# Performance work log

Measured on AMD Instinct MI355X. Metric: run time of the kernel, lower is better.

Reference implementation:

```python
import jax, jax.numpy as jnp
import numpy as np
import math

DIM = 1024
HEADS = 16
HEAD_DIM = DIM // HEADS
B, N = 1, 4096


def setup_inputs() -> dict:
    key = jax.random.key(0)
    k1, k2, k3, k4 = jax.random.split(key, 4)
    content = jax.random.normal(k1, (B, N, DIM), dtype=jnp.float32)
    # Original initializes projections as identity; perturb slightly so the
    # projections are non-trivial while staying well-conditioned.
    Wq = jnp.eye(DIM, dtype=jnp.float32) + 0.02 * jax.random.normal(k2, (DIM, DIM), dtype=jnp.float32)
    Wk = jnp.eye(DIM, dtype=jnp.float32) + 0.02 * jax.random.normal(k3, (DIM, DIM), dtype=jnp.float32)
    Wv = jnp.eye(DIM, dtype=jnp.float32) + 0.02 * jax.random.normal(k4, (DIM, DIM), dtype=jnp.float32)
    return {"content": content, "Wq": Wq, "Wk": Wk, "Wv": Wv}


def reference(content, Wq, Wk, Wv):
    b, n, d = content.shape
    # QKV projections: [B,N,D] @ [D,D]
    Q = (content @ Wq).reshape(b, n, HEADS, HEAD_DIM)
    K = (content @ Wk).reshape(b, n, HEADS, HEAD_DIM)
    V = (content @ Wv).reshape(b, n, HEADS, HEAD_DIM)
    # torch.split along the last dim == reshape into [.., HEADS, HEAD_DIM]
    scores = jnp.einsum('bqhd,bkhd->bhqk', Q, K) / math.sqrt(HEAD_DIM)
    alpha = jax.nn.softmax(scores, axis=-1)
    # Faithful to the original: masking zeroes the upper triangle AFTER the
    # softmax (no renormalization). With B=1 this applies to the whole batch,
    # exactly as the original loop (which only touches batch index 0).
    causal = jnp.tril(jnp.ones((n, n), dtype=bool))
    alpha = jnp.where(causal, alpha, jnp.zeros((), dtype=alpha.dtype))
    Y = jnp.einsum('bhqk,bkhd->bqhd', alpha, V).reshape(b, n, d)
    return Y
```

## Files before the change

### kernel.cpp

```cpp
#include <hip/hip_runtime.h>
#include <stdint.h>

#define DIMC 1024
#define NSEQ 4096
#define NH 16
#define QSCALE 0.18033688011112042f

typedef __attribute__((ext_vector_type(8))) short bf16x8;
typedef __attribute__((ext_vector_type(4))) float f32x4;

__device__ __forceinline__ unsigned short f2bf(float x) {
    union { float f; unsigned int u; } v; v.f = x;
    unsigned int u = v.u;
    return (unsigned short)((u + 0x7fffu + ((u >> 16) & 1u)) >> 16);
}

__device__ __forceinline__ unsigned cvt_pk_bf16(float lo, float hi) {
    unsigned r;
    asm("v_cvt_pk_bf16_f32 %0, %1, %2" : "=v"(r) : "v"(lo), "v"(hi));
    return r;
}

__device__ __forceinline__ void gload16(const unsigned short* g, unsigned short* l) {
    __builtin_amdgcn_global_load_lds(
        (const __attribute__((address_space(1))) void*)g,
        (__attribute__((address_space(3))) void*)l, 16, 0, 0);
}

__global__ __launch_bounds__(256) void k_conv(const float* __restrict__ in,
                                              unsigned short* __restrict__ out) {
    int i = (blockIdx.x * 256 + threadIdx.x) * 8;
    float4 a = *reinterpret_cast<const float4*>(in + i);
    float4 b = *reinterpret_cast<const float4*>(in + i + 4);
    union { unsigned short us[8]; uint4 v; } r;
    r.us[0] = f2bf(a.x); r.us[1] = f2bf(a.y); r.us[2] = f2bf(a.z); r.us[3] = f2bf(a.w);
    r.us[4] = f2bf(b.x); r.us[5] = f2bf(b.y); r.us[6] = f2bf(b.z); r.us[7] = f2bf(b.w);
    *reinterpret_cast<uint4*>(out + i) = r.v;
}

__global__ __launch_bounds__(1024) void k_wt(const float* __restrict__ Wq,
                                             const float* __restrict__ Wk,
                                             const float* __restrict__ Wv,
                                             unsigned short* __restrict__ wt) {
    __shared__ float tile[32][33];
    int z = blockIdx.z;
    const float* W = (z == 0) ? Wq : ((z == 1) ? Wk : Wv);
    int n0 = blockIdx.x * 32, k0 = blockIdx.y * 32;
    tile[threadIdx.y][threadIdx.x] = W[(k0 + threadIdx.y) * DIMC + n0 + threadIdx.x];
    __syncthreads();
    wt[(size_t)z * DIMC * DIMC + (n0 + threadIdx.y) * DIMC + k0 + threadIdx.x] =
        f2bf(tile[threadIdx.x][threadIdx.y]);
}

__global__ __launch_bounds__(256) void k_gemm(const unsigned short* __restrict__ A,
                                              const unsigned short* __restrict__ Wt,
                                              unsigned short* __restrict__ Qb,
                                              unsigned short* __restrict__ Kb,
                                              unsigned short* __restrict__ Vt) {
    __shared__ unsigned short As[128 * 32];
    __shared__ unsigned short Bs[128 * 32];
    const int z = blockIdx.z;
    const unsigned short* Wz = Wt + (size_t)z * DIMC * DIMC;
    const int n0 = blockIdx.x * 128, m0 = blockIdx.y * 128;
    const int t = threadIdx.x;
    const int w = t >> 6, l = t & 63;
    const int wr = w >> 1, wc = w & 1;
    const int lq = l & 15, lg = l >> 4;
    const int srow = l >> 2, scol = (l & 3) * 8;
    const unsigned short* gA = A  + (size_t)(m0 + w * 32 + srow) * DIMC + scol;
    const unsigned short* gB = Wz + (size_t)(n0 + w * 32 + srow) * DIMC + scol;
    unsigned short* lA = &As[(2 * w) * 512];
    unsigned short* lB = &Bs[(2 * w) * 512];

    f32x4 acc[4][4];
    #pragma unroll
    for (int i = 0; i < 4; ++i)
        #pragma unroll
        for (int j = 0; j < 4; ++j)
            acc[i][j] = f32x4{0.f, 0.f, 0.f, 0.f};

    for (int k0 = 0; k0 < DIMC; k0 += 32) {
        __syncthreads();
        gload16(gA + k0, lA);
        gload16(gA + k0 + 16 * DIMC, lA + 512);
        gload16(gB + k0, lB);
        gload16(gB + k0 + 16 * DIMC, lB + 512);
        __syncthreads();
        bf16x8 af[4], bfr[4];
        #pragma unroll
        for (int mf = 0; mf < 4; ++mf)
            af[mf] = *reinterpret_cast<const bf16x8*>(&As[(wr * 64 + mf * 16 + lq) * 32 + lg * 8]);
        #pragma unroll
        for (int nf = 0; nf < 4; ++nf)
            bfr[nf] = *reinterpret_cast<const bf16x8*>(&Bs[(wc * 64 + nf * 16 + lq) * 32 + lg * 8]);
        __builtin_amdgcn_s_setprio(1);
        #pragma unroll
        for (int mf = 0; mf < 4; ++mf)
            #pragma unroll
            for (int nf = 0; nf < 4; ++nf)
                acc[mf][nf] = __builtin_amdgcn_mfma_f32_16x16x32_bf16(af[mf], bfr[nf], acc[mf][nf], 0, 0, 0);
        __builtin_amdgcn_s_setprio(0);
    }

    if (z < 2) {
        unsigned short* out = (z == 0) ? Qb : Kb;
        const float osc = (z == 0) ? QSCALE : 1.0f;
        #pragma unroll
        for (int mf = 0; mf < 4; ++mf)
            #pragma unroll
            for (int nf = 0; nf < 4; ++nf)
                #pragma unroll
                for (int j = 0; j < 4; ++j) {
                    int row = m0 + wr * 64 + mf * 16 + lg * 4 + j;
                    int col = n0 + wc * 64 + nf * 16 + lq;
                    out[row * DIMC + col] = f2bf(acc[mf][nf][j] * osc);
                }
    } else {
        #pragma unroll
        for (int mf = 0; mf < 4; ++mf)
            #pragma unroll
            for (int nf = 0; nf < 4; ++nf) {
                int row  = n0 + wc * 64 + nf * 16 + lq;
                int colb = m0 + wr * 64 + mf * 16 + lg * 4;
                uint2 pk;
                pk.x = cvt_pk_bf16(acc[mf][nf][0], acc[mf][nf][1]);
                pk.y = cvt_pk_bf16(acc[mf][nf][2], acc[mf][nf][3]);
                *reinterpret_cast<uint2*>(Vt + (size_t)row * NSEQ + colb) = pk;
            }
    }
}

__global__ __launch_bounds__(512, 4) void k_attn(const unsigned short* __restrict__ Qb,
                                                 const unsigned short* __restrict__ Kb,
                                                 const unsigned short* __restrict__ Vt,
                                                 float* __restrict__ Y) {
    __shared__ unsigned short Ks[64][72];
    __shared__ unsigned short Vs[64][72];
    __shared__ unsigned short Ps[8][16][88];
    const int bx = blockIdx.x, h = blockIdx.y;
    const int t = threadIdx.x;
    const int w = t >> 6, l = t & 63;
    const int wq = w & 3, tile = w >> 2;
    const int lq = l & 15, lg = l >> 4;
    const int qbA = bx, qbB = 63 - bx;
    const int qb_my = tile ? qbB : qbA;

    bf16x8 qf0, qf1;
    {
        const unsigned short* qp = Qb + (size_t)(qb_my * 64 + wq * 16 + lq) * DIMC + h * 64 + lg * 8;
        qf0 = *reinterpret_cast<const bf16x8*>(qp);
        qf1 = *reinterpret_cast<const bf16x8*>(qp + 32);
    }
    float m_fr = -__builtin_inff(), l_st = 0.f;
    f32x4 O[4];
    #pragma unroll
    for (int df = 0; df < 4; ++df) O[df] = f32x4{0.f, 0.f, 0.f, 0.f};

    const int r0 = t >> 3, c0 = (t & 7) * 8;
    const unsigned short* gK = Kb + (size_t)r0 * DIMC + h * 64 + c0;
    const unsigned short* gV = Vt + (size_t)(h * 64 + r0) * NSEQ + c0;

    uint4 kv = *reinterpret_cast<const uint4*>(gK);
    uint4 vv = *reinterpret_cast<const uint4*>(gV);

    for (int kt = 0; kt < 64; ++kt) {
        __syncthreads();
        *reinterpret_cast<uint4*>(&Ks[r0][c0]) = kv;
        if (kt <= qbB) *reinterpret_cast<uint4*>(&Vs[r0][c0]) = vv;
        __syncthreads();
        if (kt < 63) {
            kv = *reinterpret_cast<const uint4*>(gK + (size_t)(kt + 1) * 64 * DIMC);
            if (kt + 1 <= qbB) vv = *reinterpret_cast<const uint4*>(gV + (kt + 1) * 64);
        }

        f32x4 s[4];
        __builtin_amdgcn_s_setprio(1);
        #pragma unroll
        for (int f = 0; f < 4; ++f) {
            s[f] = f32x4{0.f, 0.f, 0.f, 0.f};
            bf16x8 ka0 = *reinterpret_cast<const bf16x8*>(&Ks[f * 16 + lq][lg * 8]);
            bf16x8 ka1 = *reinterpret_cast<const bf16x8*>(&Ks[f * 16 + lq][32 + lg * 8]);
            s[f] = __builtin_amdgcn_mfma_f32_16x16x32_bf16(ka0, qf0, s[f], 0, 0, 0);
            s[f] = __builtin_amdgcn_mfma_f32_16x16x32_bf16(ka1, qf1, s[f], 0, 0, 0);
        }
        __builtin_amdgcn_s_setprio(0);

        float tmax = s[0][0];
        #pragma unroll
        for (int f = 0; f < 4; ++f)
            #pragma unroll
            for (int j = 0; j < 4; ++j) tmax = fmaxf(tmax, s[f][j]);
        tmax = fmaxf(tmax, __shfl_xor(tmax, 16));
        tmax = fmaxf(tmax, __shfl_xor(tmax, 32));

        if (!__all(tmax <= m_fr + 8.f)) {
            const float mnew = fmaxf(m_fr, tmax);
            const float sc = exp2f(m_fr - mnew);
            l_st *= sc;
            #pragma unroll
            for (int j = 0; j < 4; ++j) {
                const float scj = __shfl(sc, lg * 4 + j);
                #pragma unroll
                for (int df = 0; df < 4; ++df) O[df][j] *= scj;
            }
            m_fr = mnew;
        }
        float psum = 0.f;
        #pragma unroll
        for (int f = 0; f < 4; ++f)
            #pragma unroll
            for (int j = 0; j < 4; ++j) {
                const float p = exp2f(s[f][j] - m_fr);
                s[f][j] = p;
                psum += p;
            }
        psum += __shfl_xor(psum, 16);
        psum += __shfl_xor(psum, 32);
        l_st += psum;

        if (kt <= qb_my) {
            if (kt == qb_my) {
                const int qrel = wq * 16 + lq;
                #pragma unroll
                for (int f = 0; f < 4; ++f) {
                    const int kbase = f * 16 + lg * 4;
                    #pragma unroll
                    for (int j = 0; j < 4; ++j)
                        if (kbase + j > qrel) s[f][j] = 0.f;
                }
            }
            #pragma unroll
            for (int f = 0; f < 4; ++f) {
                uint2 pk;
                pk.x = cvt_pk_bf16(s[f][0], s[f][1]);
                pk.y = cvt_pk_bf16(s[f][2], s[f][3]);
                *reinterpret_cast<uint2*>(&Ps[w][lq][f * 16 + lg * 4]) = pk;
            }
            __builtin_amdgcn_s_setprio(1);
            #pragma unroll
            for (int kk = 0; kk < 2; ++kk) {
                bf16x8 pa = *reinterpret_cast<const bf16x8*>(&Ps[w][lq][kk * 32 + lg * 8]);
                #pragma unroll
                for (int df = 0; df < 4; ++df) {
                    bf16x8 vb = *reinterpret_cast<const bf16x8*>(&Vs[df * 16 + lq][kk * 32 + lg * 8]);
                    O[df] = __builtin_amdgcn_mfma_f32_16x16x32_bf16(pa, vb, O[df], 0, 0, 0);
                }
            }
            __builtin_amdgcn_s_setprio(0);
        }
    }

    const float rl = 1.0f / l_st;
    #pragma unroll
    for (int j = 0; j < 4; ++j) {
        const float li = __shfl(rl, lg * 4 + j);
        #pragma unroll
        for (int df = 0; df < 4; ++df)
            Y[(qb_my * 64 + wq * 16 + lg * 4 + j) * DIMC + h * 64 + df * 16 + lq] = O[df][j] * li;
    }
}

extern "C" void kernel_launch(void* const* d_in, const int* in_sizes, int n_in,
                              void* d_out, int out_size, void* d_ws, size_t ws_size,
                              hipStream_t stream) {
    const float* content = (const float*)d_in[0];
    const float* Wq = (const float*)d_in[1];
    const float* Wk = (const float*)d_in[2];
    const float* Wv = (const float*)d_in[3];
    float* Y = (float*)d_out;
    unsigned short* ws  = (unsigned short*)d_ws;
    unsigned short* cbf = ws;
    unsigned short* wt  = cbf + (size_t)NSEQ * DIMC;
    unsigned short* qb  = wt  + (size_t)3 * DIMC * DIMC;
    unsigned short* kb  = qb  + (size_t)NSEQ * DIMC;
    unsigned short* vt  = kb  + (size_t)NSEQ * DIMC;

    hipLaunchKernelGGL(k_conv, dim3(NSEQ * DIMC / (256 * 8)), dim3(256), 0, stream, content, cbf);
    hipLaunchKernelGGL(k_wt,   dim3(32, 32, 3), dim3(32, 32), 0, stream, Wq, Wk, Wv, wt);
    hipLaunchKernelGGL(k_gemm, dim3(DIMC / 128, NSEQ / 128, 3), dim3(256), 0, stream, cbf, wt, qb, kb, vt);
    hipLaunchKernelGGL(k_attn, dim3(NSEQ / 128, NH), dim3(512), 0, stream, qb, kb, vt, Y);
}
```

Before: 258.7 us.

## Give each attention wave two query row-groups and double-buffer K/V tiles

Cuts the attention block from 8 to 4 waves. Each wave now handles 32 query rows as two 16-row groups, so every K and V fragment read from LDS feeds two MFMAs. K/V tiles are double-buffered in shared memory with a two-step register prefetch, which removes one __syncthreads per iteration. The launch becomes a flat 1D grid with remapping so head pairs are grouped per XCD. The trade-off is more registers per wave and fewer waves to hide latency.

After: 268.9 us. 3.9% more time.

```diff
diff --git a/kernel.cpp b/kernel.cpp
--- a/kernel.cpp
+++ b/kernel.cpp
@@ -130,133 +130,184 @@
     }
 }
 
-__global__ __launch_bounds__(512, 4) void k_attn(const unsigned short* __restrict__ Qb,
-                                                 const unsigned short* __restrict__ Kb,
-                                                 const unsigned short* __restrict__ Vt,
-                                                 float* __restrict__ Y) {
-    __shared__ unsigned short Ks[64][72];
-    __shared__ unsigned short Vs[64][72];
-    __shared__ unsigned short Ps[8][16][88];
-    const int bx = blockIdx.x, h = blockIdx.y;
+__global__ __launch_bounds__(256) void k_attn(const unsigned short* __restrict__ Qb,
+                                              const unsigned short* __restrict__ Kb,
+                                              const unsigned short* __restrict__ Vt,
+                                              float* __restrict__ Y) {
+    __shared__ unsigned short Ks[2][64][72];
+    __shared__ unsigned short Vs[2][64][72];
+    __shared__ unsigned short Ps[4][32][72];
+    const int bid = blockIdx.x;
+    const int x = bid & 7, i = bid >> 3;
+    const int h = x * 2 + (i >> 5);
+    const int bx = i & 31;
     const int t = threadIdx.x;
     const int w = t >> 6, l = t & 63;
-    const int wq = w & 3, tile = w >> 2;
+    const int half = w >> 1, wq = w & 1;
     const int lq = l & 15, lg = l >> 4;
     const int qbA = bx, qbB = 63 - bx;
-    const int qb_my = tile ? qbB : qbA;
-
-    bf16x8 qf0, qf1;
-    {
-        const unsigned short* qp = Qb + (size_t)(qb_my * 64 + wq * 16 + lq) * DIMC + h * 64 + lg * 8;
-        qf0 = *reinterpret_cast<const bf16x8*>(qp);
-        qf1 = *reinterpret_cast<const bf16x8*>(qp + 32);
-    }
-    float m_fr = -__builtin_inff(), l_st = 0.f;
-    f32x4 O[4];
+    const int qb_my = half ? qbB : qbA;
+    const int vmax = qbB;
+    const int pvmax = qb_my;
+
+    bf16x8 qf[2][2];
     #pragma unroll
-    for (int df = 0; df < 4; ++df) O[df] = f32x4{0.f, 0.f, 0.f, 0.f};
+    for (int g = 0; g < 2; ++g) {
+        const unsigned short* qp = Qb + (size_t)(qb_my * 64 + wq * 32 + g * 16 + lq) * DIMC + h * 64 + lg * 8;
+        qf[g][0] = *reinterpret_cast<const bf16x8*>(qp);
+        qf[g][1] = *reinterpret_cast<const bf16x8*>(qp + 32);
+    }
+    float m_fr[2] = {-__builtin_inff(), -__builtin_inff()};
+    float l_st[2] = {0.f, 0.f};
+    f32x4 O[2][4];
+    #pragma unroll
+    for (int g = 0; g < 2; ++g)
+        #pragma unroll
+        for (int df = 0; df < 4; ++df) O[g][df] = f32x4{0.f, 0.f, 0.f, 0.f};
 
     const int r0 = t >> 3, c0 = (t & 7) * 8;
     const unsigned short* gK = Kb + (size_t)r0 * DIMC + h * 64 + c0;
     const unsigned short* gV = Vt + (size_t)(h * 64 + r0) * NSEQ + c0;
 
-    uint4 kv = *reinterpret_cast<const uint4*>(gK);
-    uint4 vv = *reinterpret_cast<const uint4*>(gV);
+    *reinterpret_cast<uint4*>(&Ks[0][r0][c0])      = *reinterpret_cast<const uint4*>(gK);
+    *reinterpret_cast<uint4*>(&Ks[0][r0 + 32][c0]) = *reinterpret_cast<const uint4*>(gK + 32 * DIMC);
+    *reinterpret_cast<uint4*>(&Vs[0][r0][c0])      = *reinterpret_cast<const uint4*>(gV);
+    *reinterpret_cast<uint4*>(&Vs[0][r0 + 32][c0]) = *reinterpret_cast<const uint4*>(gV + 32 * NSEQ);
+    uint4 kv0 = *reinterpret_cast<const uint4*>(gK + 64 * DIMC);
+    uint4 kv1 = *reinterpret_cast<const uint4*>(gK + 96 * DIMC);
+    uint4 vv0 = *reinterpret_cast<const uint4*>(gV + 64);
+    uint4 vv1 = *reinterpret_cast<const uint4*>(gV + 32 * NSEQ + 64);
 
     for (int kt = 0; kt < 64; ++kt) {
+        const int cur = kt & 1, nxt = cur ^ 1;
         __syncthreads();
-        *reinterpret_cast<uint4*>(&Ks[r0][c0]) = kv;
-        if (kt <= qbB) *reinterpret_cast<uint4*>(&Vs[r0][c0]) = vv;
-        __syncthreads();
-        if (kt < 63) {
-            kv = *reinterpret_cast<const uint4*>(gK + (size_t)(kt + 1) * 64 * DIMC);
-            if (kt + 1 <= qbB) vv = *reinterpret_cast<const uint4*>(gV + (kt + 1) * 64);
-        }
-
-        f32x4 s[4];
+        if (kt + 1 < 64) {
+            *reinterpret_cast<uint4*>(&Ks[nxt][r0][c0])      = kv0;
+            *reinterpret_cast<uint4*>(&Ks[nxt][r0 + 32][c0]) = kv1;
+            if (kt + 1 <= vmax) {
+                *reinterpret_cast<uint4*>(&Vs[nxt][r0][c0])      = vv0;
+                *reinterpret_cast<uint4*>(&Vs[nxt][r0 + 32][c0]) = vv1;
+            }
+        }
+        if (kt + 2 < 64) {
+            kv0 = *reinterpret_cast<const uint4*>(gK + (size_t)(kt + 2) * 64 * DIMC);
+            kv1 = *reinterpret_cast<const uint4*>(gK + (size_t)(kt + 2) * 64 * DIMC + 32 * DIMC);
+            if (kt + 2 <= vmax) {
+                vv0 = *reinterpret_cast<const uint4*>(gV + (kt + 2) * 64);
+                vv1 = *reinterpret_cast<const uint4*>(gV + 32 * NSEQ + (kt + 2) * 64);
+            }
+        }
+
+        f32x4 s[2][4];
+        #pragma unroll
+        for (int g = 0; g < 2; ++g)
+            #pragma unroll
+            for (int f = 0; f < 4; ++f) s[g][f] = f32x4{0.f, 0.f, 0.f, 0.f};
         __builtin_amdgcn_s_setprio(1);
         #pragma unroll
         for (int f = 0; f < 4; ++f) {
-            s[f] = f32x4{0.f, 0.f, 0.f, 0.f};
-            bf16x8 ka0 = *reinterpret_cast<const bf16x8*>(&Ks[f * 16 + lq][lg * 8]);
-            bf16x8 ka1 = *reinterpret_cast<const bf16x8*>(&Ks[f * 16 + lq][32 + lg * 8]);
-            s[f] = __builtin_amdgcn_mfma_f32_16x16x32_bf16(ka0, qf0, s[f], 0, 0, 0);
-            s[f] = __builtin_amdgcn_mfma_f32_16x16x32_bf16(ka1, qf1, s[f], 0, 0, 0);
+            bf16x8 ka0 = *reinterpret_cast<const bf16x8*>(&Ks[cur][f * 16 + lq][lg * 8]);
+            bf16x8 ka1 = *reinterpret_cast<const bf16x8*>(&Ks[cur][f * 16 + lq][32 + lg * 8]);
+            s[0][f] = __builtin_amdgcn_mfma_f32_16x16x32_bf16(ka0, qf[0][0], s[0][f], 0, 0, 0);
+            s[0][f] = __builtin_amdgcn_mfma_f32_16x16x32_bf16(ka1, qf[0][1], s[0][f], 0, 0, 0);
+            s[1][f] = __builtin_amdgcn_mfma_f32_16x16x32_bf16(ka0, qf[1][0], s[1][f], 0, 0, 0);
+            s[1][f] = __builtin_amdgcn_mfma_f32_16x16x32_bf16(ka1, qf[1][1], s[1][f], 0, 0, 0);
         }
         __builtin_amdgcn_s_setprio(0);
 
-        float tmax = s[0][0];
-        #pragma unroll
-        for (int f = 0; f < 4; ++f)
-            #pragma unroll
-            for (int j = 0; j < 4; ++j) tmax = fmaxf(tmax, s[f][j]);
-        tmax = fmaxf(tmax, __shfl_xor(tmax, 16));
-        tmax = fmaxf(tmax, __shfl_xor(tmax, 32));
-
-        if (!__all(tmax <= m_fr + 8.f)) {
-            const float mnew = fmaxf(m_fr, tmax);
-            const float sc = exp2f(m_fr - mnew);
-            l_st *= sc;
-            #pragma unroll
-            for (int j = 0; j < 4; ++j) {
-                const float scj = __shfl(sc, lg * 4 + j);
-                #pragma unroll
-                for (int df = 0; df < 4; ++df) O[df][j] *= scj;
-            }
-            m_fr = mnew;
-        }
-        float psum = 0.f;
-        #pragma unroll
-        for (int f = 0; f < 4; ++f)
-            #pragma unroll
-            for (int j = 0; j < 4; ++j) {
-                const float p = exp2f(s[f][j] - m_fr);
-                s[f][j] = p;
-                psum += p;
-            }
-        psum += __shfl_xor(psum, 16);
-        psum += __shfl_xor(psum, 32);
-        l_st += psum;
-
-        if (kt <= qb_my) {
-            if (kt == qb_my) {
-                const int qrel = wq * 16 + lq;
+        float tl[2];
+        #pragma unroll
+        for (int g = 0; g < 2; ++g) {
+            float m = s[g][0][0];
+            #pragma unroll
+            for (int f = 0; f < 4; ++f)
+                #pragma unroll
+                for (int j = 0; j < 4; ++j) m = fmaxf(m, s[g][f][j]);
+            tl[g] = m;
+        }
+        if (!__all((tl[0] <= m_fr[0] + 8.f) && (tl[1] <= m_fr[1] + 8.f))) {
+            #pragma unroll
+            for (int g = 0; g < 2; ++g) {
+                float tm = tl[g];
+                tm = fmaxf(tm, __shfl_xor(tm, 16));
+                tm = fmaxf(tm, __shfl_xor(tm, 32));
+                const float mnew = fmaxf(m_fr[g], tm);
+                const float sc = exp2f(m_fr[g] - mnew);
+                l_st[g] *= sc;
+                #pragma unroll
+                for (int j = 0; j < 4; ++j) {
+                    const float scj = __shfl(sc, lg * 4 + j);
+                    #pragma unroll
+                    for (int df = 0; df < 4; ++df) O[g][df][j] *= scj;
+                }
+                m_fr[g] = mnew;
+            }
+        }
+        #pragma unroll
+        for (int g = 0; g < 2; ++g) {
+            float ps = 0.f;
+            #pragma unroll
+            for (int f = 0; f < 4; ++f)
+                #pragma unroll
+                for (int j = 0; j < 4; ++j) {
+                    const float p = exp2f(s[g][f][j] - m_fr[g]);
+                    s[g][f][j] = p;
+                    ps += p;
+                }
+            ps += __shfl_xor(ps, 16);
+            ps += __shfl_xor(ps, 32);
+            l_st[g] += ps;
+        }
+
+        if (kt <= pvmax) {
+            if (kt == pvmax) {
+                #pragma unroll
+                for (int g = 0; g < 2; ++g) {
+                    const int qrel = wq * 32 + g * 16 + lq;
+                    #pragma unroll
+                    for (int f = 0; f < 4; ++f) {
+                        const int kbase = f * 16 + lg * 4;
+                        #pragma unroll
+                        for (int j = 0; j < 4; ++j)
+                            if (kbase + j > qrel) s[g][f][j] = 0.f;
+                    }
+                }
+            }
+            #pragma unroll
+            for (int g = 0; g < 2; ++g)
                 #pragma unroll
                 for (int f = 0; f < 4; ++f) {
-                    const int kbase = f * 16 + lg * 4;
-                    #pragma unroll
-                    for (int j = 0; j < 4; ++j)
-                        if (kbase + j > qrel) s[f][j] = 0.f;
-                }
-            }
-            #pragma unroll
-            for (int f = 0; f < 4; ++f) {
-                uint2 pk;
-                pk.x = cvt_pk_bf16(s[f][0], s[f][1]);
-                pk.y = cvt_pk_bf16(s[f][2], s[f][3]);
-                *reinterpret_cast<uint2*>(&Ps[w][lq][f * 16 + lg * 4]) = pk;
-            }
+                    uint2 pk;
+                    pk.x = cvt_pk_bf16(s[g][f][0], s[g][f][1]);
+                    pk.y = cvt_pk_bf16(s[g][f][2], s[g][f][3]);
+                    *reinterpret_cast<uint2*>(&Ps[w][g * 16 + lq][f * 16 + lg * 4]) = pk;
+                }
             __builtin_amdgcn_s_setprio(1);
             #pragma unroll
             for (int kk = 0; kk < 2; ++kk) {
-                bf16x8 pa = *reinterpret_cast<const bf16x8*>(&Ps[w][lq][kk * 32 + lg * 8]);
+                bf16x8 pa0 = *reinterpret_cast<const bf16x8*>(&Ps[w][lq][kk * 32 + lg * 8]);
+                bf16x8 pa1 = *reinterpret_cast<const bf16x8*>(&Ps[w][16 + lq][kk * 32 + lg * 8]);
                 #pragma unroll
                 for (int df = 0; df < 4; ++df) {
-                    bf16x8 vb = *reinterpret_cast<const bf16x8*>(&Vs[df * 16 + lq][kk * 32 + lg * 8]);
-                    O[df] = __builtin_amdgcn_mfma_f32_16x16x32_bf16(pa, vb, O[df], 0, 0, 0);
+                    bf16x8 vb = *reinterpret_cast<const bf16x8*>(&Vs[cur][df * 16 + lq][kk * 32 + lg * 8]);
+                    O[0][df] = __builtin_amdgcn_mfma_f32_16x16x32_bf16(pa0, vb, O[0][df], 0, 0, 0);
+                    O[1][df] = __builtin_amdgcn_mfma_f32_16x16x32_bf16(pa1, vb, O[1][df], 0, 0, 0);
                 }
             }
             __builtin_amdgcn_s_setprio(0);
         }
     }
 
-    const float rl = 1.0f / l_st;
     #pragma unroll
-    for (int j = 0; j < 4; ++j) {
-        const float li = __shfl(rl, lg * 4 + j);
-        #pragma unroll
-        for (int df = 0; df < 4; ++df)
-            Y[(qb_my * 64 + wq * 16 + lg * 4 + j) * DIMC + h * 64 + df * 16 + lq] = O[df][j] * li;
+    for (int g = 0; g < 2; ++g) {
+        const float rl = 1.0f / l_st[g];
+        #pragma unroll
+        for (int j = 0; j < 4; ++j) {
+            const float li = __shfl(rl, lg * 4 + j);
+            #pragma unroll
+            for (int df = 0; df < 4; ++df)
+                Y[(size_t)(qb_my * 64 + wq * 32 + g * 16 + lg * 4 + j) * DIMC + h * 64 + df * 16 + lq] = O[g][df][j] * li;
+        }
     }
 }
 
@@ -278,5 +329,5 @@
     hipLaunchKernelGGL(k_conv, dim3(NSEQ * DIMC / (256 * 8)), dim3(256), 0, stream, content, cbf);
     hipLaunchKernelGGL(k_wt,   dim3(32, 32, 3), dim3(32, 32), 0, stream, Wq, Wk, Wv, wt);
     hipLaunchKernelGGL(k_gemm, dim3(DIMC / 128, NSEQ / 128, 3), dim3(256), 0, stream, cbf, wt, qb, kb, vt);
-    hipLaunchKernelGGL(k_attn, dim3(NSEQ / 128, NH), dim3(512), 0, stream, qb, kb, vt, Y);
-}
+    hipLaunchKernelGGL(k_attn, dim3(512), dim3(256), 0, stream, qb, kb, vt, Y);
+}
```

## Rewrite attention with 32x32 MFMA, register P, double-buffered swizzled LDS

Applied to the files above, without the earlier changes.

The attention kernel moves from 16x16x32 to 32x32x16 bf16 MFMA tiles, with each wave owning 32 query rows. Blocks shrink to 256 threads (4 waves), and grid indices are remapped so heads are interleaved across blocks. Softmax probabilities are converted to bf16 and exchanged between lanes with cross-lane shuffles instead of a shared-memory round trip for P. K and V tiles are double-buffered in XOR-swizzled LDS, with global loads issued two tiles ahead, leaving one barrier per iteration. These changes aim to cut LDS traffic, bank conflicts and synchronisation, at the cost of more registers per thread and lower occupancy.

After: 261.7 us. Within noise of the previous version (+1.2%).

```diff
diff --git a/kernel.cpp b/kernel.cpp
--- a/kernel.cpp
+++ b/kernel.cpp
@@ -8,6 +8,7 @@
 
 typedef __attribute__((ext_vector_type(8))) short bf16x8;
 typedef __attribute__((ext_vector_type(4))) float f32x4;
+typedef __attribute__((ext_vector_type(16))) float f32x16;
 
 __device__ __forceinline__ unsigned short f2bf(float x) {
     union { float f; unsigned int u; } v; v.f = x;
@@ -130,133 +131,160 @@
     }
 }
 
-__global__ __launch_bounds__(512, 4) void k_attn(const unsigned short* __restrict__ Qb,
-                                                 const unsigned short* __restrict__ Kb,
-                                                 const unsigned short* __restrict__ Vt,
-                                                 float* __restrict__ Y) {
-    __shared__ unsigned short Ks[64][72];
-    __shared__ unsigned short Vs[64][72];
-    __shared__ unsigned short Ps[8][16][88];
-    const int bx = blockIdx.x, h = blockIdx.y;
+#define KIDX(r, c) ((r) * 64 + ((c) ^ (((r) & 7) * 8)))
+
+#define PV_STEP(SF, s16, kk) do {                                              \
+    unsigned C0a = cvt_pk_bf16(SF[8*(s16)+0], SF[8*(s16)+1]);                  \
+    unsigned C0b = cvt_pk_bf16(SF[8*(s16)+2], SF[8*(s16)+3]);                  \
+    unsigned C1a = cvt_pk_bf16(SF[8*(s16)+4], SF[8*(s16)+5]);                  \
+    unsigned C1b = cvt_pk_bf16(SF[8*(s16)+6], SF[8*(s16)+7]);                  \
+    unsigned x0 = (unsigned)__shfl_xor((int)C0a, 32);                          \
+    unsigned x2 = (unsigned)__shfl_xor((int)C0b, 32);                          \
+    unsigned x1 = (unsigned)__shfl_xor((int)C1a, 32);                          \
+    unsigned x3 = (unsigned)__shfl_xor((int)C1b, 32);                          \
+    union { uint4 u; bf16x8 b; } pcv;                                          \
+    pcv.u.x = hi ? x1 : C0a;                                                   \
+    pcv.u.y = hi ? x3 : C0b;                                                   \
+    pcv.u.z = hi ? C1a : x0;                                                   \
+    pcv.u.w = hi ? C1b : x2;                                                   \
+    bf16x8 vb0 = *reinterpret_cast<const bf16x8*>(&Vs[cur][KIDX(q32, (kk)*16 + hi*8)]);      \
+    bf16x8 vb1 = *reinterpret_cast<const bf16x8*>(&Vs[cur][KIDX(32 + q32, (kk)*16 + hi*8)]); \
+    O0 = __builtin_amdgcn_mfma_f32_32x32x16_bf16(pcv.b, vb0, O0, 0, 0, 0);     \
+    O1 = __builtin_amdgcn_mfma_f32_32x32x16_bf16(pcv.b, vb1, O1, 0, 0, 0);     \
+} while (0)
+
+__global__ __launch_bounds__(256) void k_attn(const unsigned short* __restrict__ Qb,
+                                              const unsigned short* __restrict__ Kb,
+                                              const unsigned short* __restrict__ Vt,
+                                              float* __restrict__ Y) {
+    __shared__ unsigned short Ks[2][64 * 64];
+    __shared__ unsigned short Vs[2][64 * 64];
+    const int bid = blockIdx.x;
+    const int x = bid & 7, i = bid >> 3;
+    const int h = x * 2 + (i >> 5);
+    const int bx = i & 31;
     const int t = threadIdx.x;
     const int w = t >> 6, l = t & 63;
-    const int wq = w & 3, tile = w >> 2;
-    const int lq = l & 15, lg = l >> 4;
+    const int half = w >> 1, wq = w & 1;
+    const int q32 = l & 31, hi = l >> 5;
     const int qbA = bx, qbB = 63 - bx;
-    const int qb_my = tile ? qbB : qbA;
-
-    bf16x8 qf0, qf1;
+    const int qb_my = half ? qbB : qbA;
+    const int vmax = qbB, pvmax = qb_my;
+    const int qrel = wq * 32 + q32;
+
+    bf16x8 qf[4];
     {
-        const unsigned short* qp = Qb + (size_t)(qb_my * 64 + wq * 16 + lq) * DIMC + h * 64 + lg * 8;
-        qf0 = *reinterpret_cast<const bf16x8*>(qp);
-        qf1 = *reinterpret_cast<const bf16x8*>(qp + 32);
+        const unsigned short* qp = Qb + (size_t)(qb_my * 64 + qrel) * DIMC + h * 64 + hi * 8;
+        qf[0] = *reinterpret_cast<const bf16x8*>(qp);
+        qf[1] = *reinterpret_cast<const bf16x8*>(qp + 16);
+        qf[2] = *reinterpret_cast<const bf16x8*>(qp + 32);
+        qf[3] = *reinterpret_cast<const bf16x8*>(qp + 48);
     }
     float m_fr = -__builtin_inff(), l_st = 0.f;
-    f32x4 O[4];
+    f32x16 O0, O1;
     #pragma unroll
-    for (int df = 0; df < 4; ++df) O[df] = f32x4{0.f, 0.f, 0.f, 0.f};
+    for (int j = 0; j < 16; ++j) { O0[j] = 0.f; O1[j] = 0.f; }
 
     const int r0 = t >> 3, c0 = (t & 7) * 8;
     const unsigned short* gK = Kb + (size_t)r0 * DIMC + h * 64 + c0;
     const unsigned short* gV = Vt + (size_t)(h * 64 + r0) * NSEQ + c0;
-
-    uint4 kv = *reinterpret_cast<const uint4*>(gK);
-    uint4 vv = *reinterpret_cast<const uint4*>(gV);
+    const int o_lo = KIDX(r0, c0);
+    const int o_hi = o_lo + 32 * 64;
+
+    *reinterpret_cast<uint4*>(&Ks[0][o_lo]) = *reinterpret_cast<const uint4*>(gK);
+    *reinterpret_cast<uint4*>(&Ks[0][o_hi]) = *reinterpret_cast<const uint4*>(gK + 32 * DIMC);
+    *reinterpret_cast<uint4*>(&Vs[0][o_lo]) = *reinterpret_cast<const uint4*>(gV);
+    *reinterpret_cast<uint4*>(&Vs[0][o_hi]) = *reinterpret_cast<const uint4*>(gV + 32 * NSEQ);
+    uint4 kv0 = *reinterpret_cast<const uint4*>(gK + 64 * DIMC);
+    uint4 kv1 = *reinterpret_cast<const uint4*>(gK + 96 * DIMC);
+    uint4 vv0 = *reinterpret_cast<const uint4*>(gV + 64);
+    uint4 vv1 = *reinterpret_cast<const uint4*>(gV + 32 * NSEQ + 64);
 
     for (int kt = 0; kt < 64; ++kt) {
+        const int cur = kt & 1, nxt = cur ^ 1;
         __syncthreads();
-        *reinterpret_cast<uint4*>(&Ks[r0][c0]) = kv;
-        if (kt <= qbB) *reinterpret_cast<uint4*>(&Vs[r0][c0]) = vv;
-        __syncthreads();
-        if (kt < 63) {
-            kv = *reinterpret_cast<const uint4*>(gK + (size_t)(kt + 1) * 64 * DIMC);
-            if (kt + 1 <= qbB) vv = *reinterpret_cast<const uint4*>(gV + (kt + 1) * 64);
-        }
-
-        f32x4 s[4];
+        if (kt + 1 < 64) {
+            *reinterpret_cast<uint4*>(&Ks[nxt][o_lo]) = kv0;
+            *reinterpret_cast<uint4*>(&Ks[nxt][o_hi]) = kv1;
+            if (kt + 1 <= vmax) {
+                *reinterpret_cast<uint4*>(&Vs[nxt][o_lo]) = vv0;
+                *reinterpret_cast<uint4*>(&Vs[nxt][o_hi]) = vv1;
+            }
+        }
+        if (kt + 2 < 64) {
+            kv0 = *reinterpret_cast<const uint4*>(gK + (size_t)(kt + 2) * 64 * DIMC);
+            kv1 = *reinterpret_cast<const uint4*>(gK + (size_t)(kt + 2) * 64 * DIMC + 32 * DIMC);
+            if (kt + 2 <= vmax) {
+                vv0 = *reinterpret_cast<const uint4*>(gV + (kt + 2) * 64);
+                vv1 = *reinterpret_cast<const uint4*>(gV + 32 * NSEQ + (kt + 2) * 64);
+            }
+        }
+
+        f32x16 s0, s1;
+        #pragma unroll
+        for (int j = 0; j < 16; ++j) { s0[j] = 0.f; s1[j] = 0.f; }
         __builtin_amdgcn_s_setprio(1);
         #pragma unroll
-        for (int f = 0; f < 4; ++f) {
-            s[f] = f32x4{0.f, 0.f, 0.f, 0.f};
-            bf16x8 ka0 = *reinterpret_cast<const bf16x8*>(&Ks[f * 16 + lq][lg * 8]);
-            bf16x8 ka1 = *reinterpret_cast<const bf16x8*>(&Ks[f * 16 + lq][32 + lg * 8]);
-            s[f] = __builtin_amdgcn_mfma_f32_16x16x32_bf16(ka0, qf0, s[f], 0, 0, 0);
-            s[f] = __builtin_amdgcn_mfma_f32_16x16x32_bf16(ka1, qf1, s[f], 0, 0, 0);
+        for (int c = 0; c < 4; ++c) {
+            bf16x8 ka0 = *reinterpret_cast<const bf16x8*>(&Ks[cur][KIDX(q32,      c * 16 + hi * 8)]);
+            bf16x8 ka1 = *reinterpret_cast<const bf16x8*>(&Ks[cur][KIDX(32 + q32, c * 16 + hi * 8)]);
+            s0 = __builtin_amdgcn_mfma_f32_32x32x16_bf16(ka0, qf[c], s0, 0, 0, 0);
+            s1 = __builtin_amdgcn_mfma_f32_32x32x16_bf16(ka1, qf[c], s1, 0, 0, 0);
         }
         __builtin_amdgcn_s_setprio(0);
 
-        float tmax = s[0][0];
-        #pragma unroll
-        for (int f = 0; f < 4; ++f)
-            #pragma unroll
-            for (int j = 0; j < 4; ++j) tmax = fmaxf(tmax, s[f][j]);
-        tmax = fmaxf(tmax, __shfl_xor(tmax, 16));
-        tmax = fmaxf(tmax, __shfl_xor(tmax, 32));
+        float tl = s0[0];
+        #pragma unroll
+        for (int j = 1; j < 16; ++j) tl = fmaxf(tl, s0[j]);
+        #pragma unroll
+        for (int j = 0; j < 16; ++j) tl = fmaxf(tl, s1[j]);
+        const float tmax = fmaxf(tl, __shfl_xor(tl, 32));
 
         if (!__all(tmax <= m_fr + 8.f)) {
             const float mnew = fmaxf(m_fr, tmax);
             const float sc = exp2f(m_fr - mnew);
             l_st *= sc;
             #pragma unroll
-            for (int j = 0; j < 4; ++j) {
-                const float scj = __shfl(sc, lg * 4 + j);
+            for (int j = 0; j < 16; ++j) {
+                const float scj = __shfl(sc, (j & 3) + 8 * (j >> 2) + 4 * hi);
+                O0[j] *= scj; O1[j] *= scj;
+            }
+            m_fr = mnew;
+        }
+        float ps = 0.f;
+        #pragma unroll
+        for (int j = 0; j < 16; ++j) { const float p = exp2f(s0[j] - m_fr); s0[j] = p; ps += p; }
+        #pragma unroll
+        for (int j = 0; j < 16; ++j) { const float p = exp2f(s1[j] - m_fr); s1[j] = p; ps += p; }
+        ps += __shfl_xor(ps, 32);
+        l_st += ps;
+
+        if (kt <= pvmax) {
+            if (kt == pvmax) {
                 #pragma unroll
-                for (int df = 0; df < 4; ++df) O[df][j] *= scj;
-            }
-            m_fr = mnew;
-        }
-        float psum = 0.f;
-        #pragma unroll
-        for (int f = 0; f < 4; ++f)
-            #pragma unroll
-            for (int j = 0; j < 4; ++j) {
-                const float p = exp2f(s[f][j] - m_fr);
-                s[f][j] = p;
-                psum += p;
-            }
-        psum += __shfl_xor(psum, 16);
-        psum += __shfl_xor(psum, 32);
-        l_st += psum;
-
-        if (kt <= qb_my) {
-            if (kt == qb_my) {
-                const int qrel = wq * 16 + lq;
-                #pragma unroll
-                for (int f = 0; f < 4; ++f) {
-                    const int kbase = f * 16 + lg * 4;
-                    #pragma unroll
-                    for (int j = 0; j < 4; ++j)
-                        if (kbase + j > qrel) s[f][j] = 0.f;
+                for (int j = 0; j < 16; ++j) {
+                    const int kr = (j & 3) + 8 * (j >> 2) + 4 * hi;
+                    if (kr > qrel) s0[j] = 0.f;
+                    if (32 + kr > qrel) s1[j] = 0.f;
                 }
             }
-            #pragma unroll
-            for (int f = 0; f < 4; ++f) {
-                uint2 pk;
-                pk.x = cvt_pk_bf16(s[f][0], s[f][1]);
-                pk.y = cvt_pk_bf16(s[f][2], s[f][3]);
-                *reinterpret_cast<uint2*>(&Ps[w][lq][f * 16 + lg * 4]) = pk;
-            }
             __builtin_amdgcn_s_setprio(1);
-            #pragma unroll
-            for (int kk = 0; kk < 2; ++kk) {
-                bf16x8 pa = *reinterpret_cast<const bf16x8*>(&Ps[w][lq][kk * 32 + lg * 8]);
-                #pragma unroll
-                for (int df = 0; df < 4; ++df) {
-                    bf16x8 vb = *reinterpret_cast<const bf16x8*>(&Vs[df * 16 + lq][kk * 32 + lg * 8]);
-                    O[df] = __builtin_amdgcn_mfma_f32_16x16x32_bf16(pa, vb, O[df], 0, 0, 0);
-                }
-            }
+            PV_STEP(s0, 0, 0);
+            PV_STEP(s0, 1, 1);
+            PV_STEP(s1, 0, 2);
+            PV_STEP(s1, 1, 3);
             __builtin_amdgcn_s_setprio(0);
         }
     }
 
     const float rl = 1.0f / l_st;
     #pragma unroll
-    for (int j = 0; j < 4; ++j) {
-        const float li = __shfl(rl, lg * 4 + j);
-        #pragma unroll
-        for (int df = 0; df < 4; ++df)
-            Y[(qb_my * 64 + wq * 16 + lg * 4 + j) * DIMC + h * 64 + df * 16 + lq] = O[df][j] * li;
+    for (int j = 0; j < 16; ++j) {
+        const int row = (j & 3) + 8 * (j >> 2) + 4 * hi;
+        const float rlj = __shfl(rl, row);
+        const size_t yb = (size_t)(qb_my * 64 + wq * 32 + row) * DIMC + h * 64 + q32;
+        Y[yb]      = O0[j] * rlj;
+        Y[yb + 32] = O1[j] * rlj;
     }
 }
 
@@ -278,5 +306,5 @@
     hipLaunchKernelGGL(k_conv, dim3(NSEQ * DIMC / (256 * 8)), dim3(256), 0, stream, content, cbf);
     hipLaunchKernelGGL(k_wt,   dim3(32, 32, 3), dim3(32, 32), 0, stream, Wq, Wk, Wv, wt);
     hipLaunchKernelGGL(k_gemm, dim3(DIMC / 128, NSEQ / 128, 3), dim3(256), 0, stream, cbf, wt, qb, kb, vt);
-    hipLaunchKernelGGL(k_attn, dim3(NSEQ / 128, NH), dim3(512), 0, stream, qb, kb, vt, Y);
-}
+    hipLaunchKernelGGL(k_attn, dim3(512), dim3(256), 0, stream, qb, kb, vt, Y);
+}
```
